# Optimization experiments

Measured on AMD Instinct MI355X. Metric: run time of the kernel, lower is better.

The kernel has to match this reference:

```python
import jax, jax.numpy as jnp
import numpy as np

VOCAB = 50257
EMB = 1024
H = 1024
LAYERS = 2
B = 64
S = 512


def gru_cell(x, h, w_ih, w_hh, b_ih, b_hh):
    # PyTorch GRUCell math. x:[B,in], h:[B,H], w_ih:[3H,in], w_hh:[3H,H]
    gi = x @ w_ih.T + b_ih            # [B,3H]
    gh = h @ w_hh.T + b_hh            # [B,3H]
    i_r, i_z, i_n = jnp.split(gi, 3, axis=1)
    h_r, h_z, h_n = jnp.split(gh, 3, axis=1)
    r = jax.nn.sigmoid(i_r + h_r)
    z = jax.nn.sigmoid(i_z + h_z)
    n = jnp.tanh(i_n + r * h_n)
    return (1.0 - z) * n + z * h


def setup_inputs() -> dict:
    key = jax.random.key(0)
    ks = jax.random.split(key, 16)
    s = 0.02
    inp = {
        "input_step": jax.random.randint(ks[0], (1, B), 0, VOCAB),
        "last_hidden": jax.random.normal(ks[1], (LAYERS, B, H), jnp.float32),
        "encoder_outputs": jax.random.normal(ks[2], (S, B, H), jnp.float32),
        "emb_table": jax.random.normal(ks[3], (VOCAB, EMB), jnp.float32) * s,
        "w_ih0": jax.random.normal(ks[4], (3 * H, EMB), jnp.float32) * s,
        "w_hh0": jax.random.normal(ks[5], (3 * H, H), jnp.float32) * s,
        "b_ih0": jnp.zeros((3 * H,), jnp.float32),
        "b_hh0": jnp.zeros((3 * H,), jnp.float32),
        "w_ih1": jax.random.normal(ks[6], (3 * H, H), jnp.float32) * s,
        "w_hh1": jax.random.normal(ks[7], (3 * H, H), jnp.float32) * s,
        "b_ih1": jnp.zeros((3 * H,), jnp.float32),
        "b_hh1": jnp.zeros((3 * H,), jnp.float32),
        "concat_w": jax.random.normal(ks[8], (H, 2 * H), jnp.float32) * s,
        "concat_b": jnp.zeros((H,), jnp.float32),
        "out_w": jax.random.normal(ks[9], (VOCAB, H), jnp.float32) * s,
        "out_b": jnp.zeros((VOCAB,), jnp.float32),
    }
    return inp


def reference(input_step, last_hidden, encoder_outputs, emb_table,
              w_ih0, w_hh0, b_ih0, b_hh0, w_ih1, w_hh1, b_ih1, b_hh1,
              concat_w, concat_b, out_w, out_b):
    # embedding (dropout=0 / eval mode)
    x = emb_table[input_step[0]]                       # [B,EMB]
    # 2-layer GRU, single time step
    h0 = gru_cell(x, last_hidden[0], w_ih0, w_hh0, b_ih0, b_hh0)   # [B,H]
    h1 = gru_cell(h0, last_hidden[1], w_ih1, w_hh1, b_ih1, b_hh1)  # [B,H]
    rnn_output = h1                                    # [B,H]
    hidden = jnp.stack([h0, h1], axis=0)               # [LAYERS,B,H]
    # Luong dot attention: scores [S,B] -> softmax over S per batch
    scores = jnp.einsum('bh,sbh->bs', rnn_output, encoder_outputs)  # [B,S]
    attn = jax.nn.softmax(scores, axis=1)              # [B,S]
    context = jnp.einsum('bs,sbh->bh', attn, encoder_outputs)       # [B,H]
    concat_in = jnp.concatenate([rnn_output, context], axis=1)      # [B,2H]
    concat_out = jnp.tanh(concat_in @ concat_w.T + concat_b)        # [B,H]
    logits = concat_out @ out_w.T + out_b              # [B,VOCAB]
    output = jax.nn.softmax(logits, axis=1)
    return (output, hidden)
```

## Files before the change

### kernel.cpp

```cpp
#include <hip/hip_runtime.h>
#include <hip/hip_bf16.h>
#include <math.h>

#define VOCAB 50257
#define EMB   1024
#define HID   1024
#define BATCH 64
#define SEQ   512
#define LOGITS_LD 50304
#define SCH   16
#define NCHUNK (SEQ / SCH)

typedef __attribute__((ext_vector_type(8))) short bf16x8;
typedef __attribute__((ext_vector_type(4))) float f32x4;

__device__ inline short f2bf(float x) {
    __hip_bfloat16 h = __float2bfloat16(x);
    return *reinterpret_cast<short*>(&h);
}

__device__ inline bf16x8 cvt8(const float4& a, const float4& b) {
    bf16x8 r;
    r[0] = f2bf(a.x); r[1] = f2bf(a.y); r[2] = f2bf(a.z); r[3] = f2bf(a.w);
    r[4] = f2bf(b.x); r[5] = f2bf(b.y); r[6] = f2bf(b.z); r[7] = f2bf(b.w);
    return r;
}

struct Prob {
    const void*  A;
    const int*   gidx;
    const float* W;
    const float* bias;
    float*       C;
    int N, K, ldc;
};

template <int KSLEN, int ADD_BIAS, int A_BF16>
__global__ __launch_bounds__(128, 2) void gemm_k(Prob p0, Prob p1, Prob p2)
{
    Prob P = (blockIdx.y == 0) ? p0 : ((blockIdx.y == 1) ? p1 : p2);

    const int lane = threadIdx.x & 63;
    const int wv   = threadIdx.x >> 6;
    const int rowi = lane & 15;
    const int kgi  = lane >> 4;
    const int col  = blockIdx.x * 32 + wv * 16 + rowi;
    const int wcol = min(col, P.N - 1);
    const int kbase = blockIdx.z * KSLEN + kgi * 8;

    const float* wp = P.W + (size_t)wcol * P.K + kbase;

    const float*  af[4];
    const ushort* ah[4];
#pragma unroll
    for (int mt = 0; mt < 4; ++mt) {
        int r  = rowi + mt * 16;
        int ar = P.gidx ? P.gidx[r] : r;
        af[mt] = (const float*) P.A + (size_t)ar * P.K + kbase;
        ah[mt] = (const ushort*)P.A + (size_t)ar * P.K + kbase;
    }

    f32x4 acc[4] = {};

    float4 wa0, wb0, wa1, wb1;
    bf16x8 h0b[4], h1b[4];
    float4 f0a[4], f0b[4], f1a[4], f1b[4];

    wa0 = *(const float4*)(wp);
    wb0 = *(const float4*)(wp + 4);
#pragma unroll
    for (int mt = 0; mt < 4; ++mt) {
        if (A_BF16) h0b[mt] = *(const bf16x8*)(ah[mt]);
        else { f0a[mt] = *(const float4*)(af[mt]); f0b[mt] = *(const float4*)(af[mt] + 4); }
    }
    wa1 = *(const float4*)(wp + 32);
    wb1 = *(const float4*)(wp + 36);
#pragma unroll
    for (int mt = 0; mt < 4; ++mt) {
        if (A_BF16) h1b[mt] = *(const bf16x8*)(ah[mt] + 32);
        else { f1a[mt] = *(const float4*)(af[mt] + 32); f1b[mt] = *(const float4*)(af[mt] + 36); }
    }

#pragma unroll
    for (int ks = 0; ks < KSLEN; ks += 64) {
        {
            float4 nwa = {}, nwb = {};
            bf16x8 nh[4] = {};
            float4 nfa[4] = {}, nfb[4] = {};
            if (ks + 64 < KSLEN) {
                nwa = *(const float4*)(wp + ks + 64);
                nwb = *(const float4*)(wp + ks + 68);
#pragma unroll
                for (int mt = 0; mt < 4; ++mt) {
                    if (A_BF16) nh[mt] = *(const bf16x8*)(ah[mt] + ks + 64);
                    else { nfa[mt] = *(const float4*)(af[mt] + ks + 64);
                           nfb[mt] = *(const float4*)(af[mt] + ks + 68); }
                }
            }
            bf16x8 b = cvt8(wa0, wb0);
#pragma unroll
            for (int mt = 0; mt < 4; ++mt) {
                bf16x8 a;
                if (A_BF16) a = h0b[mt]; else a = cvt8(f0a[mt], f0b[mt]);
                acc[mt] = __builtin_amdgcn_mfma_f32_16x16x32_bf16(a, b, acc[mt], 0, 0, 0);
            }
            wa0 = nwa; wb0 = nwb;
#pragma unroll
            for (int mt = 0; mt < 4; ++mt) {
                if (A_BF16) h0b[mt] = nh[mt];
                else { f0a[mt] = nfa[mt]; f0b[mt] = nfb[mt]; }
            }
        }
        {
            float4 nwa = {}, nwb = {};
            bf16x8 nh[4] = {};
            float4 nfa[4] = {}, nfb[4] = {};
            if (ks + 96 < KSLEN) {
                nwa = *(const float4*)(wp + ks + 96);
                nwb = *(const float4*)(wp + ks + 100);
#pragma unroll
                for (int mt = 0; mt < 4; ++mt) {
                    if (A_BF16) nh[mt] = *(const bf16x8*)(ah[mt] + ks + 96);
                    else { nfa[mt] = *(const float4*)(af[mt] + ks + 96);
                           nfb[mt] = *(const float4*)(af[mt] + ks + 100); }
                }
            }
            bf16x8 b = cvt8(wa1, wb1);
#pragma unroll
            for (int mt = 0; mt < 4; ++mt) {
                bf16x8 a;
                if (A_BF16) a = h1b[mt]; else a = cvt8(f1a[mt], f1b[mt]);
                acc[mt] = __builtin_amdgcn_mfma_f32_16x16x32_bf16(a, b, acc[mt], 0, 0, 0);
            }
            wa1 = nwa; wb1 = nwb;
#pragma unroll
            for (int mt = 0; mt < 4; ++mt) {
                if (A_BF16) h1b[mt] = nh[mt];
                else { f1a[mt] = nfa[mt]; f1b[mt] = nfb[mt]; }
            }
        }
    }

    if (col < P.N) {
        float bv = ADD_BIAS ? P.bias[col] : 0.0f;
        float* C = P.C + (size_t)blockIdx.z * 64 * P.ldc;
#pragma unroll
        for (int mt = 0; mt < 4; ++mt)
#pragma unroll
            for (int r = 0; r < 4; ++r) {
                int row = mt * 16 + kgi * 4 + r;
                C[(size_t)row * P.ldc + col] = acc[mt][r] + bv;
            }
    }
}

template <int NZI, int NZH>
__global__ __launch_bounds__(256) void gru_gate_k(
    const float* __restrict__ pgi, const float* __restrict__ pgh,
    const float* __restrict__ b_ih, const float* __restrict__ b_hh,
    const float* __restrict__ hprev, float* __restrict__ out_hidden,
    float* __restrict__ h_out, float* __restrict__ ci)
{
    int i = blockIdx.x * 256 + threadIdx.x;
    int b = i >> 10, j = i & 1023;
    size_t base = (size_t)b * 3072 + j;
    float ir = b_ih[j], iz = b_ih[j + 1024], in_ = b_ih[j + 2048];
    float hr = b_hh[j], hz = b_hh[j + 1024], hn  = b_hh[j + 2048];
#pragma unroll
    for (int z = 0; z < NZI; ++z) {
        size_t o = (size_t)z * 64 * 3072 + base;
        ir += pgi[o]; iz += pgi[o + 1024]; in_ += pgi[o + 2048];
    }
#pragma unroll
    for (int z = 0; z < NZH; ++z) {
        size_t o = (size_t)z * 64 * 3072 + base;
        hr += pgh[o]; hz += pgh[o + 1024]; hn  += pgh[o + 2048];
    }
    float r = 1.0f / (1.0f + expf(-(ir + hr)));
    float z = 1.0f / (1.0f + expf(-(iz + hz)));
    float n = tanhf(in_ + r * hn);
    float v = (1.0f - z) * n + z * hprev[i];
    out_hidden[i] = v;
    if (h_out) h_out[i] = v;
    if (ci)    ci[(size_t)b * 2048 + j] = v;
}

__global__ __launch_bounds__(256) void attn_fused_k(
    const float* __restrict__ h1, const float* __restrict__ enc,
    float* __restrict__ pctx, float* __restrict__ pm, float* __restrict__ ps)
{
    const int b = blockIdx.y, ck = blockIdx.x;
    __shared__ float hs[HID];
    __shared__ float es[SCH][HID];
    __shared__ float sc[SCH];
    const int tid = threadIdx.x, wv = tid >> 6, lane = tid & 63;

    ((float4*)hs)[tid] = ((const float4*)(h1 + (size_t)b * HID))[tid];
    const float* ebase = enc + ((size_t)(ck * SCH) * BATCH + b) * HID;
#pragma unroll
    for (int i = 0; i < SCH; ++i) {
        int idx = tid + i * 256;
        int r = idx >> 8, c = idx & 255;
        ((float4*)es[r])[c] = ((const float4*)(ebase + (size_t)r * BATCH * HID))[c];
    }
    __syncthreads();

#pragma unroll
    for (int i = 0; i < 4; ++i) {
        int r = wv * 4 + i;
        float acc = 0.0f;
#pragma unroll
        for (int seg = 0; seg < 4; ++seg) {
            float4 ev = ((const float4*)es[r])[lane + seg * 64];
            float4 hv = ((const float4*)hs)[lane + seg * 64];
            acc += ev.x * hv.x + ev.y * hv.y + ev.z * hv.z + ev.w * hv.w;
        }
        for (int off = 32; off; off >>= 1) acc += __shfl_down(acc, off);
        if (lane == 0) sc[r] = acc;
    }
    __syncthreads();

    float m = sc[0];
#pragma unroll
    for (int s = 1; s < SCH; ++s) m = fmaxf(m, sc[s]);
    float p[SCH];
    float sum = 0.0f;
#pragma unroll
    for (int s = 0; s < SCH; ++s) { p[s] = expf(sc[s] - m); sum += p[s]; }

    float4 cacc = {0.0f, 0.0f, 0.0f, 0.0f};
#pragma unroll
    for (int s = 0; s < SCH; ++s) {
        float4 ev = ((const float4*)es[s])[tid];
        cacc.x += p[s] * ev.x; cacc.y += p[s] * ev.y;
        cacc.z += p[s] * ev.z; cacc.w += p[s] * ev.w;
    }
    ((float4*)(pctx + ((size_t)ck * BATCH + b) * HID))[tid] = cacc;
    if (tid == 0) { pm[b * NCHUNK + ck] = m; ps[b * NCHUNK + ck] = sum; }
}

__global__ __launch_bounds__(256) void attn_comb_k(
    const float* __restrict__ pctx, const float* __restrict__ pm,
    const float* __restrict__ ps, float* __restrict__ ci)
{
    const int b = blockIdx.x, tid = threadIdx.x;
    float m = -INFINITY;
#pragma unroll
    for (int c = 0; c < NCHUNK; ++c) m = fmaxf(m, pm[b * NCHUNK + c]);
    float w[NCHUNK]; float tot = 0.0f;
#pragma unroll
    for (int c = 0; c < NCHUNK; ++c) {
        w[c] = expf(pm[b * NCHUNK + c] - m);
        tot += ps[b * NCHUNK + c] * w[c];
    }
    float inv = 1.0f / tot;
    float4 acc = {0.0f, 0.0f, 0.0f, 0.0f};
#pragma unroll
    for (int c = 0; c < NCHUNK; ++c) {
        float4 v = ((const float4*)(pctx + ((size_t)c * BATCH + b) * HID))[tid];
        acc.x += w[c] * v.x; acc.y += w[c] * v.y;
        acc.z += w[c] * v.z; acc.w += w[c] * v.w;
    }
    float4 o = {acc.x * inv, acc.y * inv, acc.z * inv, acc.w * inv};
    ((float4*)(ci + (size_t)b * 2048 + 1024))[tid] = o;
}

__global__ __launch_bounds__(256) void concat_comb_k(
    const float* __restrict__ pco, const float* __restrict__ bias,
    ushort* __restrict__ co_bf)
{
    int i = blockIdx.x * 256 + threadIdx.x;
    int j = i & 1023;
    float v = bias[j];
#pragma unroll
    for (int z = 0; z < 8; ++z) v += pco[(size_t)z * 65536 + i];
    co_bf[i] = (ushort)f2bf(tanhf(v));
}

#define VCHUNK 6284
__global__ __launch_bounds__(256) void stats_part_k(
    const float* __restrict__ logits, float* __restrict__ vmax,
    float* __restrict__ vsum, int ldc)
{
    int b = blockIdx.y, ch = blockIdx.x;
    int v0 = ch * VCHUNK;
    int v1 = min(v0 + VCHUNK, VOCAB);
    const float* row = logits + (size_t)b * ldc;
    float m = -INFINITY;
    for (int v = v0 + threadIdx.x; v < v1; v += 256) m = fmaxf(m, row[v]);
    __shared__ float red[4];
    for (int off = 32; off; off >>= 1) m = fmaxf(m, __shfl_xor(m, off));
    int wave = threadIdx.x >> 6, lane = threadIdx.x & 63;
    if (lane == 0) red[wave] = m;
    __syncthreads();
    m = fmaxf(fmaxf(red[0], red[1]), fmaxf(red[2], red[3]));
    float ssum = 0.0f;
    for (int v = v0 + threadIdx.x; v < v1; v += 256) ssum += expf(row[v] - m);
    for (int off = 32; off; off >>= 1) ssum += __shfl_xor(ssum, off);
    __syncthreads();
    if (lane == 0) red[wave] = ssum;
    __syncthreads();
    if (threadIdx.x == 0) {
        vmax[b * 8 + ch] = m;
        vsum[b * 8 + ch] = red[0] + red[1] + red[2] + red[3];
    }
}

__global__ __launch_bounds__(256) void softmax_v_k(
    const float* __restrict__ logits, const float* __restrict__ vmax,
    const float* __restrict__ vsum, float* __restrict__ out, int ldc)
{
    int b = blockIdx.y;
    float m = -INFINITY;
#pragma unroll
    for (int i = 0; i < 8; ++i) m = fmaxf(m, vmax[b * 8 + i]);
    float tot = 0.0f;
#pragma unroll
    for (int i = 0; i < 8; ++i) tot += vsum[b * 8 + i] * expf(vmax[b * 8 + i] - m);
    float inv = 1.0f / tot;
    int v = blockIdx.x * 1024 + threadIdx.x * 4;
    if (v + 3 < VOCAB) {
        float4 lv = *reinterpret_cast<const float4*>(logits + (size_t)b * ldc + v);
        float4 o;
        o.x = expf(lv.x - m) * inv; o.y = expf(lv.y - m) * inv;
        o.z = expf(lv.z - m) * inv; o.w = expf(lv.w - m) * inv;
        *reinterpret_cast<float4*>(out + (size_t)b * VOCAB + v) = o;
    } else {
        for (int k = 0; k < 4 && v + k < VOCAB; ++k)
            out[(size_t)b * VOCAB + v + k] = expf(logits[(size_t)b * ldc + v + k] - m) * inv;
    }
}

extern "C" void kernel_launch(void* const* d_in, const int* in_sizes, int n_in,
                              void* d_out, int out_size, void* d_ws, size_t ws_size,
                              hipStream_t stream)
{
    const int*   input_step  = (const int*)  d_in[0];
    const float* last_hidden = (const float*)d_in[1];
    const float* enc         = (const float*)d_in[2];
    const float* emb         = (const float*)d_in[3];
    const float* w_ih0       = (const float*)d_in[4];
    const float* w_hh0       = (const float*)d_in[5];
    const float* b_ih0       = (const float*)d_in[6];
    const float* b_hh0       = (const float*)d_in[7];
    const float* w_ih1       = (const float*)d_in[8];
    const float* w_hh1       = (const float*)d_in[9];
    const float* b_ih1       = (const float*)d_in[10];
    const float* b_hh1       = (const float*)d_in[11];
    const float* concat_w    = (const float*)d_in[12];
    const float* concat_b    = (const float*)d_in[13];
    const float* out_w       = (const float*)d_in[14];
    const float* out_b       = (const float*)d_in[15];

    float* out = (float*)d_out;
    float* out_probs  = out;
    float* out_hidden = out + (size_t)BATCH * VOCAB;

    float* ws   = (float*)d_ws;
    float* big  = ws;
    float* pgi0 = big;
    float* pgh0 = big + 786432;
    float* pgh1 = big + 1572864;
    float* pgi1 = big;
    float* pctx = big;
    float* pco  = big;
    float* logits = ws + 2359296;
    float* ci   = logits + (size_t)64 * LOGITS_LD;
    float* h0   = ci + 131072;
    float* pm   = h0 + 65536;
    float* ps   = pm + 2048;
    float* vmax = ps + 2048;
    float* vsum = vmax + 512;
    ushort* co_bf = (ushort*)(vsum + 512);

    Prob P0 = { emb,         input_step, w_ih0, nullptr, pgi0, 3 * HID, EMB, 3 * HID };
    Prob P1 = { last_hidden, nullptr,    w_hh0, nullptr, pgh0, 3 * HID, HID, 3 * HID };
    Prob P2 = { last_hidden + 64 * HID, nullptr, w_hh1, nullptr, pgh1, 3 * HID, HID, 3 * HID };

    gemm_k<256, 0, 0><<<dim3(96, 3, 4), 128, 0, stream>>>(P0, P1, P2);

    gru_gate_k<4, 4><<<256, 256, 0, stream>>>(pgi0, pgh0, b_ih0, b_hh0, last_hidden,
                                              out_hidden, h0, nullptr);

    Prob PB = { h0, nullptr, w_ih1, nullptr, pgi1, 3 * HID, HID, 3 * HID };
    gemm_k<128, 0, 0><<<dim3(96, 1, 8), 128, 0, stream>>>(PB, PB, PB);

    gru_gate_k<8, 4><<<256, 256, 0, stream>>>(pgi1, pgh1, b_ih1, b_hh1,
                                              last_hidden + 64 * HID,
                                              out_hidden + 64 * HID, nullptr, ci);

    attn_fused_k<<<dim3(NCHUNK, BATCH), 256, 0, stream>>>(
        out_hidden + 64 * HID, enc, pctx, pm, ps);
    attn_comb_k<<<BATCH, 256, 0, stream>>>(pctx, pm, ps, ci);

    Prob PC = { ci, nullptr, concat_w, nullptr, pco, HID, 2 * HID, HID };
    gemm_k<256, 0, 0><<<dim3(32, 1, 8), 128, 0, stream>>>(PC, PC, PC);
    concat_comb_k<<<256, 256, 0, stream>>>(pco, concat_b, co_bf);

    Prob PL = { co_bf, nullptr, out_w, out_b, logits, VOCAB, HID, LOGITS_LD };
    gemm_k<1024, 1, 1><<<dim3((VOCAB + 31) / 32, 1, 1), 128, 0, stream>>>(PL, PL, PL);

    stats_part_k<<<dim3(8, BATCH), 256, 0, stream>>>(logits, vmax, vsum, LOGITS_LD);
    softmax_v_k<<<dim3((VOCAB + 1023) / 1024, BATCH), 256, 0, stream>>>(
        logits, vmax, vsum, out_probs, LOGITS_LD);
}
```

Before: 201.7 us.

## Add dedicated logits GEMM streaming fp32 weights via direct global-to-LDS loads

Replaces the generic gemm_k launch for the vocab projection with a specialized kernel. Each 256-thread block covers 64 vocab rows and uses global_load_lds to stage the fp32 out_w tiles directly into a double-buffered, XOR-swizzled LDS buffer while the bf16 activations are prefetched into registers. The kernel converts weights to bf16 after reading them from LDS, feeds MFMA 16x16x32, and writes float4 outputs with bias added. The goal is to stream the large weight matrix at closer to full bandwidth and overlap loads with compute, at the cost of a __syncthreads per K step and 32KB of LDS per block, which limits occupancy.

Measured after the change: 196.9 us. 2.4% less time.

```diff
diff --git a/kernel.cpp b/kernel.cpp
--- a/kernel.cpp
+++ b/kernel.cpp
@@ -14,6 +14,9 @@
 typedef __attribute__((ext_vector_type(8))) short bf16x8;
 typedef __attribute__((ext_vector_type(4))) float f32x4;
 
+typedef const __attribute__((address_space(1))) unsigned int gu32_t;
+typedef __attribute__((address_space(3))) unsigned int lu32_t;
+
 __device__ inline short f2bf(float x) {
     __hip_bfloat16 h = __float2bfloat16(x);
     return *reinterpret_cast<short*>(&h);
@@ -151,6 +154,98 @@
                 int row = mt * 16 + kgi * 4 + r;
                 C[(size_t)row * P.ldc + col] = acc[mt][r] + bv;
             }
+    }
+}
+
+__global__ __launch_bounds__(256, 3) void logits_k(
+    const ushort* __restrict__ co_bf, const float* __restrict__ W,
+    const float* __restrict__ bias, float* __restrict__ logits)
+{
+    __shared__ float lds[2][4096];
+    const int tid  = threadIdx.x;
+    const int lane = tid & 63;
+    const int wv   = tid >> 6;
+    const int rowi = lane & 15;
+    const int kgi  = lane >> 4;
+    const int nblk = blockIdx.x * 64;
+
+    size_t srcbase[4];
+    int    ldsoff[4];
+#pragma unroll
+    for (int j = 0; j < 4; ++j) {
+        int o     = j * 4096 + tid * 16;
+        int row   = o >> 8;
+        int inner = (o & 255) ^ ((row & 7) << 5);
+        int grow  = min(nblk + row, VOCAB - 1);
+        srcbase[j] = (size_t)grow * 1024 + (inner >> 2);
+        ldsoff[j]  = (j * 4096 + wv * 1024) >> 2;
+    }
+
+    const ushort* cop = co_bf + (size_t)rowi * 1024 + kgi * 8;
+
+    f32x4 acc[4] = {};
+    bf16x8 co[2][8];
+
+#pragma unroll
+    for (int j = 0; j < 4; ++j)
+        __builtin_amdgcn_global_load_lds((gu32_t*)(W + srcbase[j]),
+                                         (lu32_t*)&lds[0][ldsoff[j]], 16, 0, 0);
+#pragma unroll
+    for (int cf = 0; cf < 4; ++cf)
+#pragma unroll
+        for (int ks = 0; ks < 2; ++ks)
+            co[0][cf * 2 + ks] = *(const bf16x8*)(cop + (size_t)cf * 16 * 1024 + ks * 32);
+    __syncthreads();
+
+    const int rloc = wv * 16 + rowi;
+    const int swz  = (rloc & 7) << 5;
+
+#pragma unroll
+    for (int t = 0; t < 16; ++t) {
+        const int cur = t & 1, nxt = cur ^ 1;
+        if (t + 1 < 16) {
+#pragma unroll
+            for (int j = 0; j < 4; ++j)
+                __builtin_amdgcn_global_load_lds(
+                    (gu32_t*)(W + srcbase[j] + (t + 1) * 64),
+                    (lu32_t*)&lds[nxt][ldsoff[j]], 16, 0, 0);
+#pragma unroll
+            for (int cf = 0; cf < 4; ++cf)
+#pragma unroll
+                for (int ks = 0; ks < 2; ++ks)
+                    co[nxt][cf * 2 + ks] = *(const bf16x8*)(
+                        cop + (size_t)cf * 16 * 1024 + (t + 1) * 64 + ks * 32);
+        }
+#pragma unroll
+        for (int ks = 0; ks < 2; ++ks) {
+            const char* p = (const char*)&lds[cur][0] + rloc * 256 +
+                            ((ks * 128 + kgi * 32) ^ swz);
+            float4 wa = *(const float4*)p;
+            float4 wb = *(const float4*)(p + 16);
+            bf16x8 wf = cvt8(wa, wb);
+#pragma unroll
+            for (int cf = 0; cf < 4; ++cf)
+                acc[cf] = __builtin_amdgcn_mfma_f32_16x16x32_bf16(
+                    wf, co[cur][cf * 2 + ks], acc[cf], 0, 0, 0);
+        }
+        __syncthreads();
+    }
+
+    const int nb = nblk + wv * 16 + kgi * 4;
+#pragma unroll
+    for (int cf = 0; cf < 4; ++cf) {
+        int b = cf * 16 + rowi;
+        if (nb + 3 < VOCAB) {
+            float4 bv = *(const float4*)(bias + nb);
+            float4 o  = {acc[cf][0] + bv.x, acc[cf][1] + bv.y,
+                         acc[cf][2] + bv.z, acc[cf][3] + bv.w};
+            *(float4*)(logits + (size_t)b * LOGITS_LD + nb) = o;
+        } else {
+#pragma unroll
+            for (int r = 0; r < 4; ++r)
+                if (nb + r < VOCAB)
+                    logits[(size_t)b * LOGITS_LD + nb + r] = acc[cf][r] + bias[nb + r];
+        }
     }
 }
 
@@ -397,8 +492,7 @@
     gemm_k<256, 0, 0><<<dim3(32, 1, 8), 128, 0, stream>>>(PC, PC, PC);
     concat_comb_k<<<256, 256, 0, stream>>>(pco, concat_b, co_bf);
 
-    Prob PL = { co_bf, nullptr, out_w, out_b, logits, VOCAB, HID, LOGITS_LD };
-    gemm_k<1024, 1, 1><<<dim3((VOCAB + 31) / 32, 1, 1), 128, 0, stream>>>(PL, PL, PL);
+    logits_k<<<(VOCAB + 63) / 64, 256, 0, stream>>>(co_bf, out_w, out_b, logits);
 
     stats_part_k<<<dim3(8, BATCH), 256, 0, stream>>>(logits, vmax, vsum, LOGITS_LD);
     softmax_v_k<<<dim3((VOCAB + 1023) / 1024, BATCH), 256, 0, stream>>>(
```

## Use persistent LDS-resident logits GEMM with fused per-slab softmax statistics

Applied to the files above, without the earlier changes.

Replaces the generic vocab-projection GEMM and the separate stats pass with a persistent kernel. Each of 256 blocks loads the whole bf16 concat output (64x1024) into swizzled LDS once via global_load_lds, then pulls 64-row slabs of out_w from an atomic work counter. Each slab's MFMA results are written out along with a partial max and sum-exp per batch row. A small reduction kernel then merges the partials, so the stats pass no longer re-reads the logits. The cost is 128KB of LDS per block, which limits occupancy to one block per CU, plus an atomic counter that must be reset in concat_comb_k.

Measured after the change: 194.4 us. 3.6% less time.

```diff
diff --git a/kernel.cpp b/kernel.cpp
--- a/kernel.cpp
+++ b/kernel.cpp
@@ -10,9 +10,13 @@
 #define LOGITS_LD 50304
 #define SCH   16
 #define NCHUNK (SEQ / SCH)
+#define NSLAB 786
 
 typedef __attribute__((ext_vector_type(8))) short bf16x8;
 typedef __attribute__((ext_vector_type(4))) float f32x4;
+
+typedef const __attribute__((address_space(1))) unsigned int gu32_t;
+typedef __attribute__((address_space(3))) unsigned int lu32_t;
 
 __device__ inline short f2bf(float x) {
     __hip_bfloat16 h = __float2bfloat16(x);
@@ -154,6 +158,157 @@
     }
 }
 
+__global__ __launch_bounds__(256) void logits_pers_k(
+    const ushort* __restrict__ co_bf, const float* __restrict__ W,
+    const float* __restrict__ bias, float* __restrict__ logits,
+    float* __restrict__ pmax, float* __restrict__ psum, int* __restrict__ ctr)
+{
+    __shared__ ushort co_s[64 * 1024];
+    __shared__ float smax[4][64], ssum[4][64];
+    __shared__ int slab_s;
+
+    const int tid  = threadIdx.x;
+    const int lane = tid & 63;
+    const int wv   = tid >> 6;
+    const int rowi = lane & 15;
+    const int kgi  = lane >> 4;
+
+#pragma unroll
+    for (int rnd = 0; rnd < 32; ++rnd) {
+        int o     = rnd * 4096 + tid * 16;
+        int row   = o >> 11;
+        int inner = o & 2047;
+        int src   = (row << 11) + (inner ^ ((row & 7) << 4));
+        __builtin_amdgcn_global_load_lds(
+            (gu32_t*)((const char*)co_bf + src),
+            (lu32_t*)(((char*)co_s) + rnd * 4096 + wv * 1024), 16, 0, 0);
+    }
+    __syncthreads();
+
+    const int rloc = wv * 16 + rowi;
+
+    while (true) {
+        if (tid == 0) slab_s = atomicAdd(ctr, 1);
+        __syncthreads();
+        const int slab = slab_s;
+        if (slab >= NSLAB) break;
+
+        const int nblk = slab * 64;
+        const int wrow = min(nblk + rloc, VOCAB - 1);
+        const float* wp = W + (size_t)wrow * 1024 + kgi * 8;
+
+        f32x4 acc[4] = {};
+        float4 wa0 = *(const float4*)(wp);
+        float4 wb0 = *(const float4*)(wp + 4);
+        float4 wa1 = *(const float4*)(wp + 32);
+        float4 wb1 = *(const float4*)(wp + 36);
+
+#pragma unroll
+        for (int s = 0; s < 32; s += 2) {
+            float4 na0 = {}, nb0 = {}, na1 = {}, nb1 = {};
+            if (s + 2 < 32) {
+                na0 = *(const float4*)(wp + (s + 2) * 32);
+                nb0 = *(const float4*)(wp + (s + 2) * 32 + 4);
+            }
+            if (s + 3 < 32) {
+                na1 = *(const float4*)(wp + (s + 3) * 32);
+                nb1 = *(const float4*)(wp + (s + 3) * 32 + 4);
+            }
+            {
+                bf16x8 wf = cvt8(wa0, wb0);
+                const int kb = s * 64 + kgi * 16;
+#pragma unroll
+                for (int cf = 0; cf < 4; ++cf) {
+                    int row = cf * 16 + rowi;
+                    const char* p = ((const char*)co_s) + row * 2048 +
+                                    (kb ^ ((row & 7) << 4));
+                    bf16x8 a = *(const bf16x8*)p;
+                    acc[cf] = __builtin_amdgcn_mfma_f32_16x16x32_bf16(wf, a, acc[cf], 0, 0, 0);
+                }
+            }
+            {
+                bf16x8 wf = cvt8(wa1, wb1);
+                const int kb = (s + 1) * 64 + kgi * 16;
+#pragma unroll
+                for (int cf = 0; cf < 4; ++cf) {
+                    int row = cf * 16 + rowi;
+                    const char* p = ((const char*)co_s) + row * 2048 +
+                                    (kb ^ ((row & 7) << 4));
+                    bf16x8 a = *(const bf16x8*)p;
+                    acc[cf] = __builtin_amdgcn_mfma_f32_16x16x32_bf16(wf, a, acc[cf], 0, 0, 0);
+                }
+            }
+            wa0 = na0; wb0 = nb0; wa1 = na1; wb1 = nb1;
+        }
+
+        const int nb = nblk + wv * 16 + kgi * 4;
+        float vals[4][4];
+#pragma unroll
+        for (int cf = 0; cf < 4; ++cf) {
+            int b = cf * 16 + rowi;
+#pragma unroll
+            for (int r = 0; r < 4; ++r)
+                vals[cf][r] = acc[cf][r] + bias[min(nb + r, VOCAB - 1)];
+            float4 o = {vals[cf][0], vals[cf][1], vals[cf][2], vals[cf][3]};
+            *(float4*)(logits + (size_t)b * LOGITS_LD + nb) = o;
+        }
+#pragma unroll
+        for (int cf = 0; cf < 4; ++cf) {
+            float m = -INFINITY;
+#pragma unroll
+            for (int r = 0; r < 4; ++r)
+                if (nb + r < VOCAB) m = fmaxf(m, vals[cf][r]);
+            m = fmaxf(m, __shfl_xor(m, 16));
+            m = fmaxf(m, __shfl_xor(m, 32));
+            float sm = 0.0f;
+#pragma unroll
+            for (int r = 0; r < 4; ++r)
+                if (nb + r < VOCAB) sm += expf(vals[cf][r] - m);
+            sm += __shfl_xor(sm, 16);
+            sm += __shfl_xor(sm, 32);
+            if (kgi == 0) { smax[wv][cf * 16 + rowi] = m; ssum[wv][cf * 16 + rowi] = sm; }
+        }
+        __syncthreads();
+        if (tid < 64) {
+            float m = fmaxf(fmaxf(smax[0][tid], smax[1][tid]),
+                            fmaxf(smax[2][tid], smax[3][tid]));
+            float t = 0.0f;
+#pragma unroll
+            for (int w = 0; w < 4; ++w) {
+                float sw = ssum[w][tid];
+                t += (sw > 0.0f) ? sw * expf(smax[w][tid] - m) : 0.0f;
+            }
+            pmax[(size_t)slab * 64 + tid] = m;
+            psum[(size_t)slab * 64 + tid] = t;
+        }
+        __syncthreads();
+    }
+}
+
+__global__ __launch_bounds__(256) void vfinal_k(
+    const float* __restrict__ pmax, const float* __restrict__ psum,
+    float* __restrict__ gm, float* __restrict__ ginv)
+{
+    const int b = blockIdx.x;
+    __shared__ float red[4];
+    float m = -INFINITY;
+    for (int s = threadIdx.x; s < NSLAB; s += 256)
+        m = fmaxf(m, pmax[(size_t)s * 64 + b]);
+    for (int off = 32; off; off >>= 1) m = fmaxf(m, __shfl_xor(m, off));
+    int wv = threadIdx.x >> 6, lane = threadIdx.x & 63;
+    if (lane == 0) red[wv] = m;
+    __syncthreads();
+    m = fmaxf(fmaxf(red[0], red[1]), fmaxf(red[2], red[3]));
+    float t = 0.0f;
+    for (int s = threadIdx.x; s < NSLAB; s += 256)
+        t += psum[(size_t)s * 64 + b] * expf(pmax[(size_t)s * 64 + b] - m);
+    for (int off = 32; off; off >>= 1) t += __shfl_xor(t, off);
+    __syncthreads();
+    if (lane == 0) red[wv] = t;
+    __syncthreads();
+    if (threadIdx.x == 0) { gm[b] = m; ginv[b] = 1.0f / (red[0] + red[1] + red[2] + red[3]); }
+}
+
 template <int NZI, int NZH>
 __global__ __launch_bounds__(256) void gru_gate_k(
     const float* __restrict__ pgi, const float* __restrict__ pgh,
@@ -267,8 +422,9 @@
 
 __global__ __launch_bounds__(256) void concat_comb_k(
     const float* __restrict__ pco, const float* __restrict__ bias,
-    ushort* __restrict__ co_bf)
-{
+    ushort* __restrict__ co_bf, int* __restrict__ ctr)
+{
+    if (blockIdx.x == 0 && threadIdx.x == 0) *ctr = 0;
     int i = blockIdx.x * 256 + threadIdx.x;
     int j = i & 1023;
     float v = bias[j];
@@ -277,57 +433,22 @@
     co_bf[i] = (ushort)f2bf(tanhf(v));
 }
 
-#define VCHUNK 6284
-__global__ __launch_bounds__(256) void stats_part_k(
-    const float* __restrict__ logits, float* __restrict__ vmax,
-    float* __restrict__ vsum, int ldc)
-{
-    int b = blockIdx.y, ch = blockIdx.x;
-    int v0 = ch * VCHUNK;
-    int v1 = min(v0 + VCHUNK, VOCAB);
-    const float* row = logits + (size_t)b * ldc;
-    float m = -INFINITY;
-    for (int v = v0 + threadIdx.x; v < v1; v += 256) m = fmaxf(m, row[v]);
-    __shared__ float red[4];
-    for (int off = 32; off; off >>= 1) m = fmaxf(m, __shfl_xor(m, off));
-    int wave = threadIdx.x >> 6, lane = threadIdx.x & 63;
-    if (lane == 0) red[wave] = m;
-    __syncthreads();
-    m = fmaxf(fmaxf(red[0], red[1]), fmaxf(red[2], red[3]));
-    float ssum = 0.0f;
-    for (int v = v0 + threadIdx.x; v < v1; v += 256) ssum += expf(row[v] - m);
-    for (int off = 32; off; off >>= 1) ssum += __shfl_xor(ssum, off);
-    __syncthreads();
-    if (lane == 0) red[wave] = ssum;
-    __syncthreads();
-    if (threadIdx.x == 0) {
-        vmax[b * 8 + ch] = m;
-        vsum[b * 8 + ch] = red[0] + red[1] + red[2] + red[3];
-    }
-}
-
 __global__ __launch_bounds__(256) void softmax_v_k(
-    const float* __restrict__ logits, const float* __restrict__ vmax,
-    const float* __restrict__ vsum, float* __restrict__ out, int ldc)
+    const float* __restrict__ logits, const float* __restrict__ gm,
+    const float* __restrict__ ginv, float* __restrict__ out)
 {
     int b = blockIdx.y;
-    float m = -INFINITY;
-#pragma unroll
-    for (int i = 0; i < 8; ++i) m = fmaxf(m, vmax[b * 8 + i]);
-    float tot = 0.0f;
-#pragma unroll
-    for (int i = 0; i < 8; ++i) tot += vsum[b * 8 + i] * expf(vmax[b * 8 + i] - m);
-    float inv = 1.0f / tot;
+    float m = gm[b], inv = ginv[b];
     int v = blockIdx.x * 1024 + threadIdx.x * 4;
     if (v + 3 < VOCAB) {
-        float4 lv = *reinterpret_cast<const float4*>(logits + (size_t)b * ldc + v);
+        float4 lv = *reinterpret_cast<const float4*>(logits + (size_t)b * LOGITS_LD + v);
         float4 o;
         o.x = expf(lv.x - m) * inv; o.y = expf(lv.y - m) * inv;
         o.z = expf(lv.z - m) * inv; o.w = expf(lv.w - m) * inv;
         *reinterpret_cast<float4*>(out + (size_t)b * VOCAB + v) = o;
     } else {
         for (int k = 0; k < 4 && v + k < VOCAB; ++k)
-            out[(size_t)b * VOCAB + v + k] = expf(logits[(size_t)b * ldc + v + k] - m) * inv;
+            out[(size_t)b * VOCAB + v + k] = expf(logits[(size_t)b * LOGITS_LD + v + k] - m) * inv;
     }
 }
 
@@ -369,9 +490,12 @@
     float* h0   = ci + 131072;
     float* pm   = h0 + 65536;
     float* ps   = pm + 2048;
-    float* vmax = ps + 2048;
-    float* vsum = vmax + 512;
-    ushort* co_bf = (ushort*)(vsum + 512);
+    float* pmax = ps + 2048;
+    float* psum = pmax + 50304;
+    float* gm   = psum + 50304;
+    float* ginv = gm + 64;
+    int*   ctr  = (int*)(ginv + 64);
+    ushort* co_bf = (ushort*)(ginv + 64 + 16);
 
     Prob P0 = { emb,         input_step, w_ih0, nullptr, pgi0, 3 * HID, EMB, 3 * HID };
     Prob P1 = { last_hidden, nullptr,    w_hh0, nullptr, pgh0, 3 * HID, HID, 3 * HID };
@@ -395,12 +519,11 @@
 
     Prob PC = { ci, nullptr, concat_w, nullptr, pco, HID, 2 * HID, HID };
     gemm_k<256, 0, 0><<<dim3(32, 1, 8), 128, 0, stream>>>(PC, PC, PC);
-    concat_comb_k<<<256, 256, 0, stream>>>(pco, concat_b, co_bf);
-
-    Prob PL = { co_bf, nullptr, out_w, out_b, logits, VOCAB, HID, LOGITS_LD };
-    gemm_k<1024, 1, 1><<<dim3((VOCAB + 31) / 32, 1, 1), 128, 0, stream>>>(PL, PL, PL);
-
-    stats_part_k<<<dim3(8, BATCH), 256, 0, stream>>>(logits, vmax, vsum, LOGITS_LD);
+    concat_comb_k<<<256, 256, 0, stream>>>(pco, concat_b, co_bf, ctr);
+
+    logits_pers_k<<<256, 256, 0, stream>>>(co_bf, out_w, out_b, logits, pmax, psum, ctr);
+
+    vfinal_k<<<BATCH, 256, 0, stream>>>(pmax, psum, gm, ginv);
     softmax_v_k<<<dim3((VOCAB + 1023) / 1024, BATCH), 256, 0, stream>>>(
-        logits, vmax, vsum, out_probs, LOGITS_LD);
-}
+        logits, gm, ginv, out_probs);
+}
```
